# Kernel tuning notes

Hardware: AMD Instinct MI355X
Metric: run time of the kernel (lower is better)

Reference implementation:

```python
import jax, jax.numpy as jnp
import numpy as np

B, N, F_IN, F_HID, F_OUT = 32, 1024, 512, 512, 512


def setup_inputs() -> dict:
    key = jax.random.key(0)
    ks = jax.random.split(key, 8)
    def xavier(k, fan_in, fan_out):
        bound = float(np.sqrt(6.0 / (fan_in + fan_out)))
        return jax.random.uniform(k, (fan_in, fan_out), jnp.float32, -bound, bound)
    return {
        "batch_graph": jax.random.normal(ks[0], (B, N, F_IN), jnp.float32),
        "adj": jax.random.uniform(ks[1], (B, N, N), jnp.float32),
        "W1": xavier(ks[2], F_IN, F_HID),
        "b1": jnp.zeros((F_HID,), jnp.float32),
        "W2": xavier(ks[3], F_HID, F_HID),
        "b2": jnp.zeros((F_HID,), jnp.float32),
        "W3": xavier(ks[4], F_HID, F_OUT),
        "b3": jnp.zeros((F_OUT,), jnp.float32),
    }


def _gcn_layer(x, adj, W, b):
    # support = X @ W ; out = A @ support + b  (per graph in the batch)
    support = jnp.einsum("bnf,fh->bnh", x, W)
    return jnp.einsum("bnm,bmh->bnh", adj, support) + b


def reference(batch_graph, adj, W1, b1, W2, b2, W3, b3):
    # Block-diagonal big_adj @ big_graph is exactly a batched per-graph matmul:
    # the zero off-diagonal blocks contribute nothing, so math is identical.
    # Dropout is identity at inference (eval mode).
    x = jax.nn.relu(_gcn_layer(batch_graph, adj, W1, b1))
    x = jax.nn.relu(_gcn_layer(x, adj, W2, b2))
    out = _gcn_layer(x, adj, W3, b3)  # [B, N, F_OUT]
    return out
```

## Files before the change

kernel.cpp:

```cpp
#include <hip/hip_runtime.h>
#include <hip/hip_bf16.h>


typedef __attribute__((ext_vector_type(8))) short bf16x8s;
typedef __attribute__((ext_vector_type(4))) float f32x4;
typedef __attribute__((ext_vector_type(4))) unsigned short us4;
typedef __attribute__((ext_vector_type(8))) unsigned short us8;

__device__ __forceinline__ unsigned short f2bf(float f) {
    unsigned u = __builtin_bit_cast(unsigned, f);
    u += 0x7fffu + ((u >> 16) & 1u);
    return (unsigned short)(u >> 16);
}

__device__ __forceinline__ void async16(const unsigned short* g, unsigned short* l) {
    __builtin_amdgcn_global_load_lds(
        (const __attribute__((address_space(1))) unsigned int*)g,
        (__attribute__((address_space(3))) unsigned int*)l, 16, 0, 0);
}

#define MFMA_(d, va, vb) d = __builtin_amdgcn_mfma_f32_16x16x32_bf16(va, vb, d, 0, 0, 0)

__global__ void prep(const float* __restrict__ x0, unsigned short* __restrict__ P0, long n4,
                     const float* __restrict__ adjf, unsigned short* __restrict__ adjb, long na4,
                     const float* __restrict__ W1, const float* __restrict__ W2,
                     const float* __restrict__ W3, unsigned short* __restrict__ WT1,
                     unsigned short* __restrict__ WT2, unsigned short* __restrict__ WT3,
                     int F) {
    long i = (long)blockIdx.x * blockDim.x + threadIdx.x;
    long stride = (long)gridDim.x * blockDim.x;
    for (long k = i; k < na4; k += stride) {
        float4 v = ((const float4*)adjf)[k];
        us4 o;
        o.x = f2bf(v.x); o.y = f2bf(v.y); o.z = f2bf(v.z); o.w = f2bf(v.w);
        ((us4*)adjb)[k] = o;
    }
    for (long k = i; k < n4; k += stride) {
        float4 v = ((const float4*)x0)[k];
        us4 o;
        o.x = f2bf(v.x); o.y = f2bf(v.y); o.z = f2bf(v.z); o.w = f2bf(v.w);
        ((us4*)P0)[k] = o;
    }
    const long FF = (long)F * F;
    for (long k = i; k < 3 * FF; k += stride) {
        int w = (int)(k / FF);
        long idx = k % FF;
        int r = (int)(idx % F);
        int c = (int)(idx / F);
        const float* W = (w == 0) ? W1 : (w == 1) ? W2 : W3;
        unsigned short* WT = (w == 0) ? WT1 : (w == 1) ? WT2 : WT3;
        WT[idx] = f2bf(W[(size_t)r * F + c]);
    }
}

template<bool RELU, bool OUT_F32>
__global__ __launch_bounds__(512, 2)
void gemm256(const unsigned short* __restrict__ A,
             const unsigned short* __restrict__ BT,
             void* __restrict__ Cout,
             const float* __restrict__ bias,
             int M, int N, int K,
             long sA, long sBT, long sC)
{
    __shared__ unsigned short Lraw[81920];

    const int t    = threadIdx.x;
    const int lane = t & 63;
    const int wv   = t >> 6;
    const int wm   = wv >> 2;
    const int wn   = wv & 3;
    const int fr   = lane & 15;
    const int fk   = (lane >> 4) * 8;
    const int r4   = (lane >> 4) * 4;

    const int tilesN = N >> 8;
    const int bpb    = (M >> 8) * tilesN;
    const int cpx = gridDim.x >> 3;
    const int lb  = (blockIdx.x & 7) * cpx + (blockIdx.x >> 3);
    const int bat = lb / bpb;
    const int tt  = lb % bpb;
    const int m0  = (tt / tilesN) << 8;
    const int n0  = (tt % tilesN) << 8;

    const unsigned short* Ab = A  + (size_t)bat * sA  + (size_t)m0 * K;
    const unsigned short* Bb = BT + (size_t)bat * sBT + (size_t)n0 * K;

    int srow[2], scol[2], lo[2];
#pragma unroll
    for (int r = 0; r < 2; ++r) {
        int c   = r * 512 + t;
        srow[r] = c >> 3;
        scol[r] = ((c & 7) * 8) ^ ((srow[r] & 7) << 3);
        lo[r]   = c * 8;
    }

    auto stageA = [&](int kt, int h) {
        unsigned short* base = Lraw + (kt & 1) * 16384;
#pragma unroll
        for (int r = 0; r < 2; ++r)
            async16(Ab + (size_t)(h * 128 + srow[r]) * K + kt * 64 + scol[r],
                    base + h * 8192 + lo[r]);
    };
    auto stageB = [&](int buf, int kt) {
        unsigned short* base = Lraw + 32768 + buf * 16384;
#pragma unroll
        for (int h = 0; h < 2; ++h)
#pragma unroll
            for (int r = 0; r < 2; ++r)
                async16(Bb + (size_t)(h * 128 + srow[r]) * K + kt * 64 + scol[r],
                        base + h * 8192 + lo[r]);
    };
    auto rdA = [&](int buf, int mf, int kkj) -> bf16x8s {
        int row = wm * 128 + mf * 16 + fr;
        int e   = (kkj * 32 + fk) ^ ((row & 7) << 3);
        return *(const bf16x8s*)&Lraw[buf * 16384 + row * 64 + e];
    };
    auto rdB = [&](int buf, int nf, int kkj) -> bf16x8s {
        int row = wn * 64 + nf * 16 + fr;
        int e   = (kkj * 32 + fk) ^ ((row & 7) << 3);
        return *(const bf16x8s*)&Lraw[32768 + buf * 16384 + row * 64 + e];
    };

    const int nt = K >> 6;

    f32x4 acc[8][4];
#pragma unroll
    for (int i = 0; i < 8; ++i)
#pragma unroll
        for (int j = 0; j < 4; ++j) acc[i][j] = f32x4{0.f, 0.f, 0.f, 0.f};

    bf16x8s aP[4], aB[4], aC[4], bX[4], bY[4];

    stageA(0, 0); stageA(0, 1);
    stageB(0, 0);
    if (nt > 1) {
        stageB(1, 1);
        asm volatile("s_waitcnt vmcnt(4)" ::: "memory");
    } else {
        asm volatile("s_waitcnt vmcnt(0)" ::: "memory");
    }
    __builtin_amdgcn_s_barrier();
#pragma unroll
    for (int m = 0; m < 4; ++m) aP[m] = rdA(0, m, 0);
#pragma unroll
    for (int n = 0; n < 4; ++n) bX[n] = rdB(0, n, 0);

    int bc = 0;
    for (int it = 0; it < nt; ++it) {
        const int cur = it & 1;
        const int bn1 = (bc == 2) ? 0 : bc + 1;
        const int bn2 = (bn1 == 2) ? 0 : bn1 + 1;
        const bool m1 = (it + 1 < nt), m2 = (it + 2 < nt);

        __builtin_amdgcn_s_barrier();
#pragma unroll
        for (int m = 0; m < 4; ++m) aB[m] = rdA(cur, m + 4, 0);
        if (m1) stageA(it + 1, 0);
        __builtin_amdgcn_s_setprio(1);
#pragma unroll
        for (int m = 0; m < 4; ++m)
#pragma unroll
            for (int n = 0; n < 4; ++n) MFMA_(acc[m][n], aP[m], bX[n]);
        __builtin_amdgcn_s_setprio(0);

        __builtin_amdgcn_s_barrier();
#pragma unroll
        for (int m = 0; m < 4; ++m) aC[m] = rdA(cur, m, 1);
#pragma unroll
        for (int n = 0; n < 4; ++n) bY[n] = rdB(bc, n, 1);
        if (m1) stageA(it + 1, 1);
        __builtin_amdgcn_s_setprio(1);
#pragma unroll
        for (int m = 0; m < 4; ++m)
#pragma unroll
            for (int n = 0; n < 4; ++n) MFMA_(acc[m + 4][n], aB[m], bX[n]);
        __builtin_amdgcn_s_setprio(0);

        __builtin_amdgcn_s_barrier();
#pragma unroll
        for (int m = 0; m < 4; ++m) aB[m] = rdA(cur, m + 4, 1);
        if (m2) stageB(bn2, it + 2);
        __builtin_amdgcn_s_setprio(1);
#pragma unroll
        for (int m = 0; m < 4; ++m)
#pragma unroll
            for (int n = 0; n < 4; ++n) MFMA_(acc[m][n], aC[m], bY[n]);
        __builtin_amdgcn_s_setprio(0);

        if (m1) {
            if (m2) asm volatile("s_waitcnt vmcnt(4)" ::: "memory");
            else    asm volatile("s_waitcnt vmcnt(0)" ::: "memory");
            __builtin_amdgcn_s_barrier();
#pragma unroll
            for (int m = 0; m < 4; ++m) aP[m] = rdA(cur ^ 1, m, 0);
#pragma unroll
            for (int n = 0; n < 4; ++n) bX[n] = rdB(bn1, n, 0);
        }
        __builtin_amdgcn_s_setprio(1);
#pragma unroll
        for (int m = 0; m < 4; ++m)
#pragma unroll
            for (int n = 0; n < 4; ++n) MFMA_(acc[m + 4][n], aB[m], bY[n]);
        __builtin_amdgcn_s_setprio(0);
        bc = bn1;
    }

    __syncthreads();

    const int R0 = m0 + wm * 128;
    const int C0 = n0 + wn * 64;
    float bv[4];
#pragma unroll
    for (int j = 0; j < 4; ++j)
        bv[j] = bias ? bias[C0 + j * 16 + fr] : 0.f;

    if (OUT_F32) {
        float* Cb = (float*)Cout + (size_t)bat * sC;
#pragma unroll
        for (int j = 0; j < 4; ++j)
#pragma unroll
            for (int i = 0; i < 8; ++i)
#pragma unroll
                for (int e = 0; e < 4; ++e) {
                    float v = acc[i][j][e] + bv[j];
                    if (RELU) v = fmaxf(v, 0.f);
                    Cb[(size_t)(R0 + i * 16 + r4 + e) * N + C0 + j * 16 + fr] = v;
                }
    } else {
        unsigned short* sl = Lraw + wv * 8192;
#pragma unroll
        for (int i = 0; i < 8; ++i)
#pragma unroll
            for (int j = 0; j < 4; ++j)
#pragma unroll
                for (int e = 0; e < 4; ++e) {
                    float v = acc[i][j][e] + bv[j];
                    if (RELU) v = fmaxf(v, 0.f);
                    const int row = i * 16 + r4 + e;
                    const int col = j * 16 + fr;
                    sl[row * 64 + (col ^ ((row & 7) << 3))] = f2bf(v);
                }
        unsigned short* Cb = (unsigned short*)Cout + (size_t)bat * sC;
#pragma unroll
        for (int rr = 0; rr < 16; ++rr) {
            const int row = rr * 8 + (lane >> 3);
            const int k8  = lane & 7;
            us8 v = *(const us8*)&sl[row * 64 + ((k8 ^ (row & 7)) << 3)];
            *(us8*)&Cb[(size_t)(R0 + row) * N + C0 + k8 * 8] = v;
        }
    }
}

extern "C" void kernel_launch(void* const* d_in, const int* in_sizes, int n_in,
                              void* d_out, int out_size, void* d_ws, size_t ws_size,
                              hipStream_t stream) {
    constexpr int B = 32, N = 1024, F = 512;

    const float* x0f  = (const float*)d_in[0];
    const float* adjf = (const float*)d_in[1];
    const float* W1 = (const float*)d_in[2];
    const float* b1 = (const float*)d_in[3];
    const float* W2 = (const float*)d_in[4];
    const float* b2 = (const float*)d_in[5];
    const float* W3 = (const float*)d_in[6];
    const float* b3 = (const float*)d_in[7];

    unsigned short* ws   = (unsigned short*)d_ws;
    unsigned short* adjb = ws;
    unsigned short* P0   = adjb + (size_t)B * N * N;
    unsigned short* P1   = P0 + (size_t)B * N * F;
    unsigned short* PT   = P1 + (size_t)B * N * F;
    unsigned short* WT1  = PT + (size_t)B * N * F;
    unsigned short* WT2  = WT1 + (size_t)F * F;
    unsigned short* WT3  = WT2 + (size_t)F * F;

    prep<<<2048, 256, 0, stream>>>(x0f, P0, (long)B * N * F / 4,
                                   adjf, adjb, (long)B * N * N / 4,
                                   W1, W2, W3, WT1, WT2, WT3, F);

    const int grid = 256;
    const long sX = (long)N * F;
    const long sAd = (long)N * N;

    gemm256<false, false><<<grid, 512, 0, stream>>>(WT1,  P0, PT, nullptr, F, N, F, 0,  sX, sX);
    gemm256<true,  false><<<grid, 512, 0, stream>>>(adjb, PT, P1, b1,      N, F, N, sAd, sX, sX);
    gemm256<false, false><<<grid, 512, 0, stream>>>(WT2,  P1, PT, nullptr, F, N, F, 0,  sX, sX);
    gemm256<true,  false><<<grid, 512, 0, stream>>>(adjb, PT, P0, b2,      N, F, N, sAd, sX, sX);
    gemm256<false, false><<<grid, 512, 0, stream>>>(WT3,  P0, PT, nullptr, F, N, F, 0,  sX, sX);
    gemm256<false, true ><<<grid, 512, 0, stream>>>(adjb, PT, (float*)d_out, b3, N, F, N, sAd, sX, sX);
}
```

Baseline: 256.0 us.

## Fuse fp32-to-bf16 conversion of inputs and adjacency into first-layer GEMMs

The separate prep pass that converted the full fp32 feature tensor and the adjacency to bf16 is removed. The first X·W GEMM now reads fp32 features directly and packs them to bf16 in registers before writing LDS. The first adj·support GEMM does the same with the fp32 adjacency, and its n0==0 blocks also write the bf16 copy to the workspace for the later layers. This cuts one full read and write of the large adjacency tensor, at the cost of fp32 register staging and more global traffic inside the GEMM main loops.

```diff
diff --git a/kernel.cpp b/kernel.cpp
--- a/kernel.cpp
+++ b/kernel.cpp
@@ -13,6 +13,13 @@
     return (unsigned short)(u >> 16);
 }
 
+__device__ __forceinline__ us8 pack8(float4 a, float4 b) {
+    us8 o;
+    o[0] = f2bf(a.x); o[1] = f2bf(a.y); o[2] = f2bf(a.z); o[3] = f2bf(a.w);
+    o[4] = f2bf(b.x); o[5] = f2bf(b.y); o[6] = f2bf(b.z); o[7] = f2bf(b.w);
+    return o;
+}
+
 __device__ __forceinline__ void async16(const unsigned short* g, unsigned short* l) {
     __builtin_amdgcn_global_load_lds(
         (const __attribute__((address_space(1))) unsigned int*)g,
@@ -21,28 +28,13 @@
 
 #define MFMA_(d, va, vb) d = __builtin_amdgcn_mfma_f32_16x16x32_bf16(va, vb, d, 0, 0, 0)
 
-__global__ void prep(const float* __restrict__ x0, unsigned short* __restrict__ P0, long n4,
-                     const float* __restrict__ adjf, unsigned short* __restrict__ adjb, long na4,
-                     const float* __restrict__ W1, const float* __restrict__ W2,
+__global__ void prep(const float* __restrict__ W1, const float* __restrict__ W2,
                      const float* __restrict__ W3, unsigned short* __restrict__ WT1,
-                     unsigned short* __restrict__ WT2, unsigned short* __restrict__ WT3,
-                     int F) {
-    long i = (long)blockIdx.x * blockDim.x + threadIdx.x;
-    long stride = (long)gridDim.x * blockDim.x;
-    for (long k = i; k < na4; k += stride) {
-        float4 v = ((const float4*)adjf)[k];
-        us4 o;
-        o.x = f2bf(v.x); o.y = f2bf(v.y); o.z = f2bf(v.z); o.w = f2bf(v.w);
-        ((us4*)adjb)[k] = o;
-    }
-    for (long k = i; k < n4; k += stride) {
-        float4 v = ((const float4*)x0)[k];
-        us4 o;
-        o.x = f2bf(v.x); o.y = f2bf(v.y); o.z = f2bf(v.z); o.w = f2bf(v.w);
-        ((us4*)P0)[k] = o;
-    }
+                     unsigned short* __restrict__ WT2, unsigned short* __restrict__ WT3) {
+    constexpr int F = 512;
     const long FF = (long)F * F;
-    for (long k = i; k < 3 * FF; k += stride) {
+    const long S = (long)gridDim.x * 256;
+    for (long k = (long)blockIdx.x * 256 + threadIdx.x; k < 3 * FF; k += S) {
         int w = (int)(k / FF);
         long idx = k % FF;
         int r = (int)(idx % F);
@@ -50,6 +42,343 @@
         const float* W = (w == 0) ? W1 : (w == 1) ? W2 : W3;
         unsigned short* WT = (w == 0) ? WT1 : (w == 1) ? WT2 : WT3;
         WT[idx] = f2bf(W[(size_t)r * F + c]);
+    }
+}
+
+__global__ __launch_bounds__(512, 2)
+void gemm_g1f(const unsigned short* __restrict__ WT,
+              const float* __restrict__ X0,
+              unsigned short* __restrict__ PT)
+{
+    constexpr int K = 512, NN = 1024;
+    constexpr int nt = K >> 6;
+    __shared__ unsigned short Lraw[65536];
+
+    const int t = threadIdx.x, lane = t & 63, wv = t >> 6;
+    const int wm = wv >> 2, wn = wv & 3;
+    const int fr = lane & 15, fk = (lane >> 4) * 8, r4 = (lane >> 4) * 4;
+    const int lb = ((int)blockIdx.x & 7) * 32 + ((int)blockIdx.x >> 3);
+    const int bat = lb >> 3, tt = lb & 7;
+    const int m0 = (tt >> 2) << 8, n0 = (tt & 3) << 8;
+
+    const unsigned short* Ab = WT + (size_t)m0 * K;
+    const float* Bb = X0 + (size_t)bat * NN * K + (size_t)n0 * K;
+
+    int srow[2], scol[2], lo[2];
+#pragma unroll
+    for (int r = 0; r < 2; ++r) {
+        int c   = r * 512 + t;
+        srow[r] = c >> 3;
+        scol[r] = ((c & 7) * 8) ^ ((srow[r] & 7) << 3);
+        lo[r]   = c * 8;
+    }
+
+    auto stageA = [&](int kt, int h) {
+        unsigned short* base = Lraw + (kt & 1) * 16384;
+#pragma unroll
+        for (int r = 0; r < 2; ++r)
+            async16(Ab + (size_t)(h * 128 + srow[r]) * K + kt * 64 + scol[r],
+                    base + h * 8192 + lo[r]);
+    };
+    auto rdA = [&](int buf, int mf, int kkj) -> bf16x8s {
+        int row = wm * 128 + mf * 16 + fr;
+        int e   = (kkj * 32 + fk) ^ ((row & 7) << 3);
+        return *(const bf16x8s*)&Lraw[buf * 16384 + row * 64 + e];
+    };
+    auto rdB = [&](int buf, int nf, int kkj) -> bf16x8s {
+        int row = wn * 64 + nf * 16 + fr;
+        int e   = (kkj * 32 + fk) ^ ((row & 7) << 3);
+        return *(const bf16x8s*)&Lraw[32768 + buf * 16384 + row * 64 + e];
+    };
+
+    float4 fa[4], fb[4];
+    auto loadB = [&](int kt) {
+#pragma unroll
+        for (int h = 0; h < 2; ++h)
+#pragma unroll
+            for (int r = 0; r < 2; ++r) {
+                const float* p = Bb + (size_t)(h * 128 + srow[r]) * K + kt * 64 + scol[r];
+                fa[h * 2 + r] = *(const float4*)p;
+                fb[h * 2 + r] = *(const float4*)(p + 4);
+            }
+    };
+    auto writeB = [&](int buf) {
+#pragma unroll
+        for (int h = 0; h < 2; ++h)
+#pragma unroll
+            for (int r = 0; r < 2; ++r)
+                *(us8*)&Lraw[32768 + buf * 16384 + h * 8192 + lo[r]] =
+                    pack8(fa[h * 2 + r], fb[h * 2 + r]);
+    };
+
+    f32x4 acc[8][4];
+#pragma unroll
+    for (int i = 0; i < 8; ++i)
+#pragma unroll
+        for (int j = 0; j < 4; ++j) acc[i][j] = f32x4{0.f, 0.f, 0.f, 0.f};
+    bf16x8s aP[4], aB[4], aC[4], bX[4], bY[4];
+
+    loadB(0);
+    stageA(0, 0); stageA(0, 1);
+    writeB(0);
+    loadB(1);
+    __syncthreads();
+#pragma unroll
+    for (int m = 0; m < 4; ++m) aP[m] = rdA(0, m, 0);
+#pragma unroll
+    for (int n = 0; n < 4; ++n) bX[n] = rdB(0, n, 0);
+
+    for (int it = 0; it < nt; ++it) {
+        const int cur = it & 1, nxt = cur ^ 1;
+        const bool m1 = it + 1 < nt, m2 = it + 2 < nt;
+
+        __builtin_amdgcn_s_barrier();
+#pragma unroll
+        for (int m = 0; m < 4; ++m) aB[m] = rdA(cur, m + 4, 0);
+        if (m1) stageA(it + 1, 0);
+        __builtin_amdgcn_s_setprio(1);
+#pragma unroll
+        for (int m = 0; m < 4; ++m)
+#pragma unroll
+            for (int n = 0; n < 4; ++n) MFMA_(acc[m][n], aP[m], bX[n]);
+        __builtin_amdgcn_s_setprio(0);
+
+        __builtin_amdgcn_s_barrier();
+#pragma unroll
+        for (int m = 0; m < 4; ++m) aC[m] = rdA(cur, m, 1);
+#pragma unroll
+        for (int n = 0; n < 4; ++n) bY[n] = rdB(cur, n, 1);
+        if (m1) stageA(it + 1, 1);
+        __builtin_amdgcn_s_setprio(1);
+#pragma unroll
+        for (int m = 0; m < 4; ++m)
+#pragma unroll
+            for (int n = 0; n < 4; ++n) MFMA_(acc[m + 4][n], aB[m], bX[n]);
+        __builtin_amdgcn_s_setprio(0);
+
+        __builtin_amdgcn_s_barrier();
+#pragma unroll
+        for (int m = 0; m < 4; ++m) aB[m] = rdA(cur, m + 4, 1);
+        if (m1) writeB(nxt);
+        __builtin_amdgcn_s_setprio(1);
+#pragma unroll
+        for (int m = 0; m < 4; ++m)
+#pragma unroll
+            for (int n = 0; n < 4; ++n) MFMA_(acc[m][n], aC[m], bY[n]);
+        __builtin_amdgcn_s_setprio(0);
+
+        if (m1) {
+            asm volatile("s_waitcnt vmcnt(0) lgkmcnt(0)" ::: "memory");
+            __builtin_amdgcn_s_barrier();
+#pragma unroll
+            for (int m = 0; m < 4; ++m) aP[m] = rdA(nxt, m, 0);
+#pragma unroll
+            for (int n = 0; n < 4; ++n) bX[n] = rdB(nxt, n, 0);
+            if (m2) loadB(it + 2);
+        }
+        __builtin_amdgcn_s_setprio(1);
+#pragma unroll
+        for (int m = 0; m < 4; ++m)
+#pragma unroll
+            for (int n = 0; n < 4; ++n) MFMA_(acc[m + 4][n], aB[m], bY[n]);
+        __builtin_amdgcn_s_setprio(0);
+    }
+
+    __syncthreads();
+    const int R0 = m0 + wm * 128;
+    const int C0 = n0 + wn * 64;
+    unsigned short* sl = Lraw + wv * 8192;
+#pragma unroll
+    for (int i = 0; i < 8; ++i)
+#pragma unroll
+        for (int j = 0; j < 4; ++j)
+#pragma unroll
+            for (int e = 0; e < 4; ++e) {
+                const int row = i * 16 + r4 + e;
+                const int col = j * 16 + fr;
+                sl[row * 64 + (col ^ ((row & 7) << 3))] = f2bf(acc[i][j][e]);
+            }
+    unsigned short* Cb = PT + (size_t)bat * 512 * 1024;
+#pragma unroll
+    for (int rr = 0; rr < 16; ++rr) {
+        const int row = rr * 8 + (lane >> 3);
+        const int k8  = lane & 7;
+        us8 v = *(const us8*)&sl[row * 64 + ((k8 ^ (row & 7)) << 3)];
+        *(us8*)&Cb[(size_t)(R0 + row) * NN + C0 + k8 * 8] = v;
+    }
+}
+
+__global__ __launch_bounds__(512, 2)
+void gemm_g2f(const float* __restrict__ ADJ,
+              unsigned short* __restrict__ adjb,
+              const unsigned short* __restrict__ PT,
+              unsigned short* __restrict__ P1,
+              const float* __restrict__ bias)
+{
+    constexpr int K = 1024, NN = 512;
+    constexpr int nt = K >> 6;
+    __shared__ unsigned short Lraw[65536];
+
+    const int t = threadIdx.x, lane = t & 63, wv = t >> 6;
+    const int wm = wv >> 2, wn = wv & 3;
+    const int fr = lane & 15, fk = (lane >> 4) * 8, r4 = (lane >> 4) * 4;
+    const int lb = ((int)blockIdx.x & 7) * 32 + ((int)blockIdx.x >> 3);
+    const int bat = lb >> 3, tt = lb & 7;
+    const int m0 = (tt >> 1) << 8, n0 = (tt & 1) << 8;
+    const bool wb = (n0 == 0);
+
+    const float* Afb = ADJ + (size_t)bat * K * K + (size_t)m0 * K;
+    unsigned short* Awb = adjb + (size_t)bat * K * K + (size_t)m0 * K;
+    const unsigned short* Bb = PT + (size_t)bat * NN * K + (size_t)n0 * K;
+
+    int srow[2], scol[2], lo[2];
+#pragma unroll
+    for (int r = 0; r < 2; ++r) {
+        int c   = r * 512 + t;
+        srow[r] = c >> 3;
+        scol[r] = ((c & 7) * 8) ^ ((srow[r] & 7) << 3);
+        lo[r]   = c * 8;
+    }
+
+    auto stageB = [&](int kt, int h) {
+        unsigned short* base = Lraw + 32768 + (kt & 1) * 16384;
+#pragma unroll
+        for (int r = 0; r < 2; ++r)
+            async16(Bb + (size_t)(h * 128 + srow[r]) * K + kt * 64 + scol[r],
+                    base + h * 8192 + lo[r]);
+    };
+    auto rdA = [&](int buf, int mf, int kkj) -> bf16x8s {
+        int row = wm * 128 + mf * 16 + fr;
+        int e   = (kkj * 32 + fk) ^ ((row & 7) << 3);
+        return *(const bf16x8s*)&Lraw[buf * 16384 + row * 64 + e];
+    };
+    auto rdB = [&](int buf, int nf, int kkj) -> bf16x8s {
+        int row = wn * 64 + nf * 16 + fr;
+        int e   = (kkj * 32 + fk) ^ ((row & 7) << 3);
+        return *(const bf16x8s*)&Lraw[32768 + buf * 16384 + row * 64 + e];
+    };
+
+    float4 fa[4], fb[4];
+    auto loadA = [&](int kt) {
+#pragma unroll
+        for (int h = 0; h < 2; ++h)
+#pragma unroll
+            for (int r = 0; r < 2; ++r) {
+                const float* p = Afb + (size_t)(h * 128 + srow[r]) * K + kt * 64 + scol[r];
+                fa[h * 2 + r] = *(const float4*)p;
+                fb[h * 2 + r] = *(const float4*)(p + 4);
+            }
+    };
+    auto flushA = [&](int buf, int kt) {
+#pragma unroll
+        for (int h = 0; h < 2; ++h)
+#pragma unroll
+            for (int r = 0; r < 2; ++r) {
+                us8 v = pack8(fa[h * 2 + r], fb[h * 2 + r]);
+                *(us8*)&Lraw[buf * 16384 + h * 8192 + lo[r]] = v;
+                if (wb)
+                    *(us8*)&Awb[(size_t)(h * 128 + srow[r]) * K + kt * 64 + scol[r]] = v;
+            }
+    };
+
+    f32x4 acc[8][4];
+#pragma unroll
+    for (int i = 0; i < 8; ++i)
+#pragma unroll
+        for (int j = 0; j < 4; ++j) acc[i][j] = f32x4{0.f, 0.f, 0.f, 0.f};
+    bf16x8s aP[4], aB[4], aC[4], bX[4], bY[4];
+
+    loadA(0);
+    stageB(0, 0); stageB(0, 1);
+    flushA(0, 0);
+    loadA(1);
+    __syncthreads();
+#pragma unroll
+    for (int m = 0; m < 4; ++m) aP[m] = rdA(0, m, 0);
+#pragma unroll
+    for (int n = 0; n < 4; ++n) bX[n] = rdB(0, n, 0);
+
+    for (int it = 0; it < nt; ++it) {
+        const int cur = it & 1, nxt = cur ^ 1;
+        const bool m1 = it + 1 < nt, m2 = it + 2 < nt;
+
+        __builtin_amdgcn_s_barrier();
+#pragma unroll
+        for (int m = 0; m < 4; ++m) aB[m] = rdA(cur, m + 4, 0);
+        if (m1) stageB(it + 1, 0);
+        __builtin_amdgcn_s_setprio(1);
+#pragma unroll
+        for (int m = 0; m < 4; ++m)
+#pragma unroll
+            for (int n = 0; n < 4; ++n) MFMA_(acc[m][n], aP[m], bX[n]);
+        __builtin_amdgcn_s_setprio(0);
+
+        __builtin_amdgcn_s_barrier();
+#pragma unroll
+        for (int m = 0; m < 4; ++m) aC[m] = rdA(cur, m, 1);
+#pragma unroll
+        for (int n = 0; n < 4; ++n) bY[n] = rdB(cur, n, 1);
+        if (m1) stageB(it + 1, 1);
+        __builtin_amdgcn_s_setprio(1);
+#pragma unroll
+        for (int m = 0; m < 4; ++m)
+#pragma unroll
+            for (int n = 0; n < 4; ++n) MFMA_(acc[m + 4][n], aB[m], bX[n]);
+        __builtin_amdgcn_s_setprio(0);
+
+        __builtin_amdgcn_s_barrier();
+#pragma unroll
+        for (int m = 0; m < 4; ++m) aB[m] = rdA(cur, m + 4, 1);
+        if (m1) flushA(nxt, it + 1);
+        __builtin_amdgcn_s_setprio(1);
+#pragma unroll
+        for (int m = 0; m < 4; ++m)
+#pragma unroll
+            for (int n = 0; n < 4; ++n) MFMA_(acc[m][n], aC[m], bY[n]);
+        __builtin_amdgcn_s_setprio(0);
+
+        if (m1) {
+            asm volatile("s_waitcnt vmcnt(0) lgkmcnt(0)" ::: "memory");
+            __builtin_amdgcn_s_barrier();
+#pragma unroll
+            for (int m = 0; m < 4; ++m) aP[m] = rdA(nxt, m, 0);
+#pragma unroll
+            for (int n = 0; n < 4; ++n) bX[n] = rdB(nxt, n, 0);
+            if (m2) loadA(it + 2);
+        }
+        __builtin_amdgcn_s_setprio(1);
+#pragma unroll
+        for (int m = 0; m < 4; ++m)
+#pragma unroll
+            for (int n = 0; n < 4; ++n) MFMA_(acc[m + 4][n], aB[m], bY[n]);
+        __builtin_amdgcn_s_setprio(0);
+    }
+
+    __syncthreads();
+    const int R0 = m0 + wm * 128;
+    const int C0 = n0 + wn * 64;
+    float bv[4];
+#pragma unroll
+    for (int j = 0; j < 4; ++j) bv[j] = bias[C0 + j * 16 + fr];
+    unsigned short* sl = Lraw + wv * 8192;
+#pragma unroll
+    for (int i = 0; i < 8; ++i)
+#pragma unroll
+        for (int j = 0; j < 4; ++j)
+#pragma unroll
+            for (int e = 0; e < 4; ++e) {
+                const int row = i * 16 + r4 + e;
+                const int col = j * 16 + fr;
+                sl[row * 64 + (col ^ ((row & 7) << 3))] =
+                    f2bf(fmaxf(acc[i][j][e] + bv[j], 0.f));
+            }
+    unsigned short* Cb = P1 + (size_t)bat * 1024 * 512;
+#pragma unroll
+    for (int rr = 0; rr < 16; ++rr) {
+        const int row = rr * 8 + (lane >> 3);
+        const int k8  = lane & 7;
+        us8 v = *(const us8*)&sl[row * 64 + ((k8 ^ (row & 7)) << 3)];
+        *(us8*)&Cb[(size_t)(R0 + row) * NN + C0 + k8 * 8] = v;
     }
 }
 
@@ -274,16 +603,14 @@
     unsigned short* WT2  = WT1 + (size_t)F * F;
     unsigned short* WT3  = WT2 + (size_t)F * F;
 
-    prep<<<2048, 256, 0, stream>>>(x0f, P0, (long)B * N * F / 4,
-                                   adjf, adjb, (long)B * N * N / 4,
-                                   W1, W2, W3, WT1, WT2, WT3, F);
+    prep<<<256, 256, 0, stream>>>(W1, W2, W3, WT1, WT2, WT3);
 
     const int grid = 256;
     const long sX = (long)N * F;
     const long sAd = (long)N * N;
 
-    gemm256<false, false><<<grid, 512, 0, stream>>>(WT1,  P0, PT, nullptr, F, N, F, 0,  sX, sX);
-    gemm256<true,  false><<<grid, 512, 0, stream>>>(adjb, PT, P1, b1,      N, F, N, sAd, sX, sX);
+    gemm_g1f<<<grid, 512, 0, stream>>>(WT1, x0f, PT);
+    gemm_g2f<<<grid, 512, 0, stream>>>(adjf, adjb, PT, P1, b1);
     gemm256<false, false><<<grid, 512, 0, stream>>>(WT2,  P1, PT, nullptr, F, N, F, 0,  sX, sX);
     gemm256<true,  false><<<grid, 512, 0, stream>>>(adjb, PT, P0, b2,      N, F, N, sAd, sX, sX);
     gemm256<false, false><<<grid, 512, 0, stream>>>(WT3,  P0, PT, nullptr, F, N, F, 0,  sX, sX);
```

Measured after the change: 239.0 us. 6.6% less time.
